# Kernel optimization log

Measured on AMD Instinct MI355X. Metric: run time of the kernel, lower is better.

## Reference

```python
import jax, jax.numpy as jnp
import numpy as np

B, S, DIM, RANK = 2, 1024, 256, 32


def setup_inputs() -> dict:
    key = jax.random.key(0)
    k_x, k_A, k_W = jax.random.split(key, 3)
    x = jax.random.normal(k_x, (B, S, DIM), dtype=jnp.float32)
    A = jax.random.normal(k_A, (RANK, DIM), dtype=jnp.float32) * 0.02
    log_lambda = jnp.log(jnp.asarray(0.1, dtype=jnp.float32))
    # position_mod Linear(dim, rank): W [rank, dim], b [rank]
    bound = 1.0 / np.sqrt(DIM)
    W = jax.random.uniform(k_W, (RANK, DIM), minval=-bound, maxval=bound, dtype=jnp.float32)
    b = jnp.zeros((RANK,), dtype=jnp.float32)
    return {"x": x, "A": A, "log_lambda": log_lambda, "W": W, "b": b}


def reference(x, A, log_lambda, W, b):
    # mod = tanh(Linear(x)): [b, s, rank]
    mod = jnp.tanh(jnp.einsum('bsd,rd->bsr', x, W) + b)
    # A_mod[b,s,r,i] = A[r,i] * mod[b,s,r]
    A_mod = mod[..., None] * A  # [b, s, rank, dim]
    # g = sum_r A_mod[...,r,i] * A_mod[...,r,j] : position-modulated low-rank Gram
    g = jnp.einsum('bsri,bsrj->bsij', A_mod, A_mod)  # [b, s, dim, dim]
    lam = jnp.exp(log_lambda)
    eye = jnp.eye(A.shape[1], dtype=g.dtype)
    return g + lam * eye
```

## Files before the change

### kernel.cpp

```cpp
#include <hip/hip_runtime.h>
#include <math.h>


constexpr int DIM  = 256;
constexpr int RANK = 32;

typedef float f32x4 __attribute__((ext_vector_type(4)));
typedef short s16x8 __attribute__((ext_vector_type(8)));

static __device__ __forceinline__ unsigned short f2bf(float f) {
    unsigned int u = __builtin_bit_cast(unsigned int, f);
    u = (u + 0x7FFFu + ((u >> 16) & 1u)) >> 16;
    return (unsigned short)u;
}

__global__ __launch_bounds__(256) void build_vt_kernel(
    const float* __restrict__ x, const float* __restrict__ A,
    const float* __restrict__ W, const float* __restrict__ bvec,
    unsigned short* __restrict__ vt_g)
{
    __shared__ float xs[DIM];
    __shared__ float sw[RANK];
    const int tid = threadIdx.x, pos = blockIdx.x;

    xs[tid] = x[(size_t)pos * DIM + tid];
    __syncthreads();

    {
        const int r = tid >> 3, seg = tid & 7;
        const f32x4* wr4 = (const f32x4*)(W + r * DIM + seg * 32);
        const f32x4* xr4 = (const f32x4*)(xs + seg * 32);
        float dot = 0.f;
        #pragma unroll
        for (int qq = 0; qq < 8; ++qq) {
            f32x4 wv = wr4[qq], xv = xr4[qq];
            dot = fmaf(wv.x, xv.x, dot);
            dot = fmaf(wv.y, xv.y, dot);
            dot = fmaf(wv.z, xv.z, dot);
            dot = fmaf(wv.w, xv.w, dot);
        }
        dot += __shfl_xor(dot, 1);
        dot += __shfl_xor(dot, 2);
        dot += __shfl_xor(dot, 4);
        if (seg == 0) sw[r] = tanhf(dot + bvec[r]);
    }
    __syncthreads();

    #pragma unroll
    for (int kg = 0; kg < 4; ++kg) {
        s16x8 pk;
        #pragma unroll
        for (int e = 0; e < 8; ++e) {
            const int k = kg * 8 + e;
            pk[e] = (short)f2bf(sw[k] * A[k * DIM + tid]);
        }
        *(s16x8*)&vt_g[(((size_t)pos * 4 + kg) * DIM + tid) * 8] = pk;
    }
}

__global__ __launch_bounds__(256) void store_g_kernel(
    const unsigned short* __restrict__ vt_g,
    const float* __restrict__ log_lambda,
    float* __restrict__ out)
{
    __shared__ alignas(16) float stage[4][16 * 128];

    const int tid  = threadIdx.x;
    const int pos  = blockIdx.x;
    const int lane = tid & 63;
    const int rs   = tid >> 6;
    const int kg   = lane >> 4, cl = lane & 15;

    const unsigned short* vbase = vt_g + ((size_t)pos * 4 + kg) * DIM * 8;

    s16x8 afr[4];
    #pragma unroll
    for (int t = 0; t < 4; ++t)
        afr[t] = *(const s16x8*)&vbase[(size_t)((4 * rs + t) * 16 + cl) * 8];

    const float lam = expf(log_lambda[0]);
    const bool on_diag_lane = (kg == (cl >> 2));
    const int  diag_slot    = cl & 3;

    float* sbuf = stage[rs];
    const int wbase = cl * 128 + 4 * kg;
    const int wswz  = (cl & 7) << 2;
    const int rrow0 = lane >> 5;
    const int rcol  = (lane & 31) * 4;

    float* gbase = out + (size_t)pos * DIM * DIM;

    #pragma unroll 1
    for (int t = 0; t < 4; ++t) {
        #pragma unroll 1
        for (int half = 0; half < 2; ++half) {
            s16x8 bfr[8];
            #pragma unroll
            for (int uu = 0; uu < 8; ++uu) {
                const int u = half * 8 + uu;
                bfr[uu] = *(const s16x8*)&vbase[(size_t)(u * 16 + cl) * 8];
            }
            #pragma unroll
            for (int uu = 0; uu < 8; ++uu) {
                const int u = half * 8 + uu;
                f32x4 acc = (f32x4)(0.f);
                acc = __builtin_amdgcn_mfma_f32_16x16x32_bf16(bfr[uu], afr[t], acc, 0, 0, 0);
                if (u == rs * 4 + t && on_diag_lane)
                    acc[diag_slot] += lam;
                *(f32x4*)&sbuf[(wbase + uu * 16) ^ wswz] = acc;
            }
            #pragma unroll
            for (int m = 0; m < 8; ++m) {
                const int row = 2 * m + rrow0;
                f32x4 v = *(const f32x4*)&sbuf[(row * 128 + rcol) ^ ((row & 7) << 2)];
                float* gp = gbase + (size_t)(rs * 64 + t * 16 + row) * DIM
                                  + half * 128 + rcol;
                __builtin_nontemporal_store(v, (f32x4*)gp);
            }
        }
    }
}

__global__ __launch_bounds__(256, 2) void riemannian_metric_fallback(
    const float* __restrict__ x, const float* __restrict__ A,
    const float* __restrict__ log_lambda, const float* __restrict__ W,
    const float* __restrict__ bvec, float* __restrict__ out)
{
    __shared__ float xs[DIM];
    __shared__ float sw[RANK];
    __shared__ alignas(16) unsigned short vt[4][DIM][8];
    __shared__ alignas(16) float stage[4][16 * 128];

    const int tid  = threadIdx.x;
    const int pos  = blockIdx.x;
    const int lane = tid & 63;
    const int rs   = tid >> 6;

    xs[tid] = x[(size_t)pos * DIM + tid];
    __syncthreads();
    {
        const int r = tid >> 3, seg = tid & 7;
        const f32x4* wr4 = (const f32x4*)(W + r * DIM + seg * 32);
        const f32x4* xr4 = (const f32x4*)(xs + seg * 32);
        float dot = 0.f;
        #pragma unroll
        for (int qq = 0; qq < 8; ++qq) {
            f32x4 wv = wr4[qq], xv = xr4[qq];
            dot = fmaf(wv.x, xv.x, dot);
            dot = fmaf(wv.y, xv.y, dot);
            dot = fmaf(wv.z, xv.z, dot);
            dot = fmaf(wv.w, xv.w, dot);
        }
        dot += __shfl_xor(dot, 1);
        dot += __shfl_xor(dot, 2);
        dot += __shfl_xor(dot, 4);
        if (seg == 0) sw[r] = tanhf(dot + bvec[r]);
    }
    __syncthreads();
    #pragma unroll
    for (int g = 0; g < 4; ++g) {
        s16x8 pk;
        #pragma unroll
        for (int e = 0; e < 8; ++e) {
            const int k = g * 8 + e;
            pk[e] = (short)f2bf(sw[k] * A[k * DIM + tid]);
        }
        *(s16x8*)&vt[g][tid][0] = pk;
    }
    __syncthreads();

    const int kg = lane >> 4, cl = lane & 15;
    s16x8 bfr[16];
    #pragma unroll
    for (int u = 0; u < 16; ++u)
        bfr[u] = *(const s16x8*)&vt[kg][u * 16 + cl][0];
    s16x8 afr[4];
    #pragma unroll
    for (int t = 0; t < 4; ++t)
        afr[t] = *(const s16x8*)&vt[kg][rs * 64 + t * 16 + cl][0];

    const float lam = expf(log_lambda[0]);
    const bool on_diag_lane = (kg == (cl >> 2));
    const int  diag_slot    = cl & 3;

    float* sbuf = stage[rs];
    const int wbase = cl * 128 + 4 * kg;
    const int wswz  = (cl & 7) << 2;
    const int rrow0 = lane >> 5;
    const int rcol  = (lane & 31) * 4;
    float* gbase = out + (size_t)pos * DIM * DIM;

    #pragma unroll 1
    for (int t = 0; t < 4; ++t) {
        #pragma unroll 1
        for (int half = 0; half < 2; ++half) {
            #pragma unroll
            for (int uu = 0; uu < 8; ++uu) {
                const int u = half * 8 + uu;
                f32x4 acc = (f32x4)(0.f);
                acc = __builtin_amdgcn_mfma_f32_16x16x32_bf16(bfr[u], afr[t], acc, 0, 0, 0);
                if (u == rs * 4 + t && on_diag_lane)
                    acc[diag_slot] += lam;
                *(f32x4*)&sbuf[(wbase + uu * 16) ^ wswz] = acc;
            }
            #pragma unroll
            for (int m = 0; m < 8; ++m) {
                const int row = 2 * m + rrow0;
                f32x4 v = *(const f32x4*)&sbuf[(row * 128 + rcol) ^ ((row & 7) << 2)];
                float* gp = gbase + (size_t)(rs * 64 + t * 16 + row) * DIM
                                  + half * 128 + rcol;
                __builtin_nontemporal_store(v, (f32x4*)gp);
            }
        }
    }
}

extern "C" void kernel_launch(void* const* d_in, const int* in_sizes, int n_in,
                              void* d_out, int out_size, void* d_ws, size_t ws_size,
                              hipStream_t stream) {
    const float* x          = (const float*)d_in[0];
    const float* A          = (const float*)d_in[1];
    const float* log_lambda = (const float*)d_in[2];
    const float* W          = (const float*)d_in[3];
    const float* bvec       = (const float*)d_in[4];
    float* out              = (float*)d_out;

    const int n_pos = in_sizes[0] / DIM;
    const size_t vt_bytes = (size_t)n_pos * 4 * DIM * 8 * sizeof(unsigned short);

    if (ws_size >= vt_bytes) {
        unsigned short* vt_g = (unsigned short*)d_ws;
        build_vt_kernel<<<n_pos, 256, 0, stream>>>(x, A, W, bvec, vt_g);
        store_g_kernel<<<n_pos, 256, 0, stream>>>(vt_g, log_lambda, out);
    } else {
        riemannian_metric_fallback<<<n_pos, 256, 0, stream>>>(x, A, log_lambda, W, bvec, out);
    }
}
```

Before: 127.3 us.

## Fold squared modulation into one operand and share a single bf16 A

Rather than writing a per-position scaled bf16 copy of A to the workspace, the first kernel now stores only the squared tanh modulation per position (32 floats), plus one shared bf16 copy of A made by an extra block. The Gram kernel scales only its A-side fragments by mod^2 and reads the unscaled shared A for the B side, using g = A^T diag(mod^2) A. This cuts workspace traffic sharply (a 16 KB per-position intermediate becomes 128 B) and makes the B operand loads hit a small cached buffer. The cost is a double bf16 rounding on one operand, which changes numerics slightly.

```diff
diff --git a/kernel.cpp b/kernel.cpp
--- a/kernel.cpp
+++ b/kernel.cpp
@@ -2,8 +2,7 @@
 #include <math.h>
 
 
-constexpr int DIM  = 256;
-constexpr int RANK = 32;
+constexpr int DIM = 256;
 
 typedef float f32x4 __attribute__((ext_vector_type(4)));
 typedef short s16x8 __attribute__((ext_vector_type(8)));
@@ -13,53 +12,57 @@
     u = (u + 0x7FFFu + ((u >> 16) & 1u)) >> 16;
     return (unsigned short)u;
 }
-
-__global__ __launch_bounds__(256) void build_vt_kernel(
+static __device__ __forceinline__ float bf2f(unsigned short s) {
+    return __builtin_bit_cast(float, (unsigned int)s << 16);
+}
+
+__global__ __launch_bounds__(256) void build_sw2_kernel(
     const float* __restrict__ x, const float* __restrict__ A,
     const float* __restrict__ W, const float* __restrict__ bvec,
-    unsigned short* __restrict__ vt_g)
+    float* __restrict__ sw2, unsigned short* __restrict__ ab16, int n_pos)
 {
+    const int tid = threadIdx.x, b = blockIdx.x;
+
+    if (b == n_pos) {
+        #pragma unroll
+        for (int kg = 0; kg < 4; ++kg) {
+            s16x8 pk;
+            #pragma unroll
+            for (int e = 0; e < 8; ++e)
+                pk[e] = (short)f2bf(A[(kg * 8 + e) * DIM + tid]);
+            *(s16x8*)&ab16[((size_t)kg * DIM + tid) * 8] = pk;
+        }
+        return;
+    }
+
     __shared__ float xs[DIM];
-    __shared__ float sw[RANK];
-    const int tid = threadIdx.x, pos = blockIdx.x;
-
-    xs[tid] = x[(size_t)pos * DIM + tid];
-    __syncthreads();
-
-    {
-        const int r = tid >> 3, seg = tid & 7;
-        const f32x4* wr4 = (const f32x4*)(W + r * DIM + seg * 32);
-        const f32x4* xr4 = (const f32x4*)(xs + seg * 32);
-        float dot = 0.f;
-        #pragma unroll
-        for (int qq = 0; qq < 8; ++qq) {
-            f32x4 wv = wr4[qq], xv = xr4[qq];
-            dot = fmaf(wv.x, xv.x, dot);
-            dot = fmaf(wv.y, xv.y, dot);
-            dot = fmaf(wv.z, xv.z, dot);
-            dot = fmaf(wv.w, xv.w, dot);
-        }
-        dot += __shfl_xor(dot, 1);
-        dot += __shfl_xor(dot, 2);
-        dot += __shfl_xor(dot, 4);
-        if (seg == 0) sw[r] = tanhf(dot + bvec[r]);
-    }
-    __syncthreads();
-
-    #pragma unroll
-    for (int kg = 0; kg < 4; ++kg) {
-        s16x8 pk;
-        #pragma unroll
-        for (int e = 0; e < 8; ++e) {
-            const int k = kg * 8 + e;
-            pk[e] = (short)f2bf(sw[k] * A[k * DIM + tid]);
-        }
-        *(s16x8*)&vt_g[(((size_t)pos * 4 + kg) * DIM + tid) * 8] = pk;
+    xs[tid] = x[(size_t)b * DIM + tid];
+    __syncthreads();
+
+    const int r = tid >> 3, seg = tid & 7;
+    const f32x4* wr4 = (const f32x4*)(W + r * DIM + seg * 32);
+    const f32x4* xr4 = (const f32x4*)(xs + seg * 32);
+    float dot = 0.f;
+    #pragma unroll
+    for (int qq = 0; qq < 8; ++qq) {
+        f32x4 wv = wr4[qq], xv = xr4[qq];
+        dot = fmaf(wv.x, xv.x, dot);
+        dot = fmaf(wv.y, xv.y, dot);
+        dot = fmaf(wv.z, xv.z, dot);
+        dot = fmaf(wv.w, xv.w, dot);
+    }
+    dot += __shfl_xor(dot, 1);
+    dot += __shfl_xor(dot, 2);
+    dot += __shfl_xor(dot, 4);
+    if (seg == 0) {
+        float m = tanhf(dot + bvec[r]);
+        sw2[(size_t)b * 32 + r] = m * m;
     }
 }
 
 __global__ __launch_bounds__(256) void store_g_kernel(
-    const unsigned short* __restrict__ vt_g,
+    const unsigned short* __restrict__ ab16,
+    const float* __restrict__ sw2,
     const float* __restrict__ log_lambda,
     float* __restrict__ out)
 {
@@ -71,12 +74,21 @@
     const int rs   = tid >> 6;
     const int kg   = lane >> 4, cl = lane & 15;
 
-    const unsigned short* vbase = vt_g + ((size_t)pos * 4 + kg) * DIM * 8;
+    const unsigned short* abase = ab16 + (size_t)kg * DIM * 8;
+
+    const float* w2p = sw2 + (size_t)pos * 32 + kg * 8;
+    f32x4 w2lo = *(const f32x4*)w2p;
+    f32x4 w2hi = *(const f32x4*)(w2p + 4);
+    float w2v[8] = {w2lo.x, w2lo.y, w2lo.z, w2lo.w, w2hi.x, w2hi.y, w2hi.z, w2hi.w};
 
     s16x8 afr[4];
     #pragma unroll
-    for (int t = 0; t < 4; ++t)
-        afr[t] = *(const s16x8*)&vbase[(size_t)((4 * rs + t) * 16 + cl) * 8];
+    for (int t = 0; t < 4; ++t) {
+        s16x8 ar = *(const s16x8*)&abase[(size_t)((4 * rs + t) * 16 + cl) * 8];
+        #pragma unroll
+        for (int e = 0; e < 8; ++e)
+            afr[t][e] = (short)f2bf(w2v[e] * bf2f((unsigned short)ar[e]));
+    }
 
     const float lam = expf(log_lambda[0]);
     const bool on_diag_lane = (kg == (cl >> 2));
@@ -98,7 +110,7 @@
             #pragma unroll
             for (int uu = 0; uu < 8; ++uu) {
                 const int u = half * 8 + uu;
-                bfr[uu] = *(const s16x8*)&vbase[(size_t)(u * 16 + cl) * 8];
+                bfr[uu] = *(const s16x8*)&abase[(size_t)(u * 16 + cl) * 8];
             }
             #pragma unroll
             for (int uu = 0; uu < 8; ++uu) {
@@ -127,7 +139,7 @@
     const float* __restrict__ bvec, float* __restrict__ out)
 {
     __shared__ float xs[DIM];
-    __shared__ float sw[RANK];
+    __shared__ float sw[32];
     __shared__ alignas(16) unsigned short vt[4][DIM][8];
     __shared__ alignas(16) float stage[4][16 * 128];
 
@@ -226,12 +238,14 @@
     float* out              = (float*)d_out;
 
     const int n_pos = in_sizes[0] / DIM;
-    const size_t vt_bytes = (size_t)n_pos * 4 * DIM * 8 * sizeof(unsigned short);
-
-    if (ws_size >= vt_bytes) {
-        unsigned short* vt_g = (unsigned short*)d_ws;
-        build_vt_kernel<<<n_pos, 256, 0, stream>>>(x, A, W, bvec, vt_g);
-        store_g_kernel<<<n_pos, 256, 0, stream>>>(vt_g, log_lambda, out);
+    const size_t ab16_bytes = (size_t)4 * DIM * 8 * sizeof(unsigned short);
+    const size_t need = ab16_bytes + (size_t)n_pos * 32 * sizeof(float);
+
+    if (ws_size >= need) {
+        unsigned short* ab16 = (unsigned short*)d_ws;
+        float* sw2 = (float*)((char*)d_ws + ab16_bytes);
+        build_sw2_kernel<<<n_pos + 1, 256, 0, stream>>>(x, A, W, bvec, sw2, ab16, n_pos);
+        store_g_kernel<<<n_pos, 256, 0, stream>>>(ab16, sw2, log_lambda, out);
     } else {
         riemannian_metric_fallback<<<n_pos, 256, 0, stream>>>(x, A, log_lambda, W, bvec, out);
     }
```

Result: faster. 118.0 us (-7.3%).
